# Performance work log

Hardware: AMD Instinct MI355X
Metric: run time of the kernel (lower is better)

The kernel has to match this reference:

```python
import jax, jax.numpy as jnp
import numpy as np

N = 50000   # nodes
E = 800000  # edges (avg degree 16)
D = 128     # dim (in == out per layer)
R = 8       # num_relations
B = 4       # num_bases
L = 2       # conv_layer_num
EPS = 1e-5      # LayerNorm eps
SLOPE = 0.2     # leaky_relu negative slope


def setup_inputs() -> dict:
    key = jax.random.key(0)
    ks = jax.random.split(key, 10)
    s = 0.05
    x = jax.random.normal(ks[0], (N, D), dtype=jnp.float32)
    edge_index = jax.random.randint(ks[1], (2, E), 0, N)
    edge_type = jax.random.randint(ks[2], (E,), 0, R)
    basis = jax.random.normal(ks[3], (L, B, D, D), dtype=jnp.float32) * s
    att_r = jax.random.normal(ks[4], (L, R, B), dtype=jnp.float32) * s
    att = jax.random.normal(ks[5], (L, 2 * D), dtype=jnp.float32) * s
    root = jax.random.normal(ks[6], (L, D, D), dtype=jnp.float32) * s
    bias = jax.random.normal(ks[7], (L, D), dtype=jnp.float32) * s
    ln_w = jnp.ones((L, D), dtype=jnp.float32)
    ln_b = jnp.zeros((L, D), dtype=jnp.float32)
    return {"x": x, "edge_index": edge_index, "edge_type": edge_type,
            "basis": basis, "att_r": att_r, "att": att, "root": root,
            "bias": bias, "ln_w": ln_w, "ln_b": ln_b}


def _gnn_layer(x, src, dst, et, basis, att_r, att, root, bias, ln_w, ln_b):
    # relation weights from bases: [R, D, D]
    w = jnp.einsum('rb,bio->rio', att_r, basis)
    # transform all nodes under all relations once, then gather per edge
    xw = jnp.einsum('ni,rio->rno', x, w)          # [R, N, D]
    x_j = xw[et, src]                              # [E, D] relation-specific src msg
    xr = x @ root                                  # [N, D] root transform
    x_i = xr[dst]                                  # [E, D]
    # attention: (cat[x_i, x_j] * att).sum(-1), leaky_relu, segment softmax by dst
    alpha = x_i @ att[:D] + x_j @ att[D:]          # [E]
    alpha = jnp.where(alpha > 0, alpha, SLOPE * alpha)
    amax = jax.ops.segment_max(alpha, dst, num_segments=N)
    amax = jnp.where(jnp.isfinite(amax), amax, 0.0)
    ex = jnp.exp(alpha - amax[dst])
    denom = jax.ops.segment_sum(ex, dst, num_segments=N)
    alpha = ex / (denom[dst] + 1e-16)
    # weighted scatter-add aggregation (dropout rate = 0 -> identity)
    aggr = jax.ops.segment_sum(x_j * alpha[:, None], dst, num_segments=N)  # [N, D]
    out = aggr + xr + bias
    # LayerNorm
    mu = out.mean(-1, keepdims=True)
    var = out.var(-1, keepdims=True)
    out = (out - mu) / jnp.sqrt(var + EPS) * ln_w + ln_b
    return jnp.tanh(out)


def reference(x, edge_index, edge_type, basis, att_r, att, root, bias, ln_w, ln_b):
    src, dst = edge_index[0], edge_index[1]
    states = []
    for l in range(L):
        x = _gnn_layer(x, src, dst, edge_type, basis[l], att_r[l], att[l],
                       root[l], bias[l], ln_w[l], ln_b[l])
        states.append(x)
    return (x, jnp.stack(states))
```

## Files before the change

kernel.cpp:

```cpp
#include <hip/hip_runtime.h>
#include <math.h>

#define D 128
#define NB 4
#define NR 8
#define NLAYER 2
#define KTOT 640
#define EPSV 1e-5f
#define SLOPE 0.2f
#define NBUK 32
#define BSHIFT 11

typedef __attribute__((ext_vector_type(8))) short short8;
typedef __attribute__((ext_vector_type(4))) float f32x4;
typedef __attribute__((ext_vector_type(2))) float f32x2;

__device__ __forceinline__ unsigned short f2bf(float f) {
  unsigned u = __float_as_uint(f);
  u += 0x7FFF + ((u >> 16) & 1);
  return (unsigned short)(u >> 16);
}

__device__ __forceinline__ float block_sum_128(float v, volatile float* scratch) {
#pragma unroll
  for (int off = 32; off > 0; off >>= 1) v += __shfl_xor(v, off);
  __syncthreads();
  if ((threadIdx.x & 63) == 0) scratch[threadIdx.x >> 6] = v;
  __syncthreads();
  return scratch[0] + scratch[1];
}

__global__ void hist_kernel(const int* __restrict__ dst, int* __restrict__ deg, int E) {
  int e = blockIdx.x * 256 + threadIdx.x;
  if (e < E) atomicAdd(&deg[dst[e]], 1);
}

__global__ void __launch_bounds__(1024) scan_kernel(const int* __restrict__ deg,
                                                    int* __restrict__ offs,
                                                    int* __restrict__ cur,
                                                    int* __restrict__ bcur, int n) {
  __shared__ int wsums[16];
  const int tid = threadIdx.x, lane = tid & 63, wid = tid >> 6;
  int carry = 0;
  for (int base = 0; base < n; base += 4096) {
    int i0 = base + tid * 4;
    int v0 = 0, v1 = 0, v2 = 0, v3 = 0;
    if (i0 + 3 < n) {
      int4 q = *(const int4*)(deg + i0);
      v0 = q.x; v1 = q.y; v2 = q.z; v3 = q.w;
    } else if (i0 < n) {
      v0 = deg[i0];
      if (i0 + 1 < n) v1 = deg[i0 + 1];
      if (i0 + 2 < n) v2 = deg[i0 + 2];
    }
    int tsum = v0 + v1 + v2 + v3;
    int x = tsum;
#pragma unroll
    for (int off = 1; off < 64; off <<= 1) {
      int y = __shfl_up(x, off);
      if (lane >= off) x += y;
    }
    if (lane == 63) wsums[wid] = x;
    __syncthreads();
    if (wid == 0) {
      int ws = (lane < 16) ? wsums[lane] : 0;
#pragma unroll
      for (int off = 1; off < 16; off <<= 1) {
        int y = __shfl_up(ws, off);
        if (lane >= off) ws += y;
      }
      if (lane < 16) wsums[lane] = ws;
    }
    __syncthreads();
    int prefix = carry + ((wid > 0) ? wsums[wid - 1] : 0) + x - tsum;
    int e0 = prefix, e1 = e0 + v0, e2 = e1 + v1, e3 = e2 + v2;
    if (i0 < n)     { offs[i0] = e0;     cur[i0] = e0; }
    if (i0 + 1 < n) { offs[i0 + 1] = e1; cur[i0 + 1] = e1; }
    if (i0 + 2 < n) { offs[i0 + 2] = e2; cur[i0 + 2] = e2; }
    if (i0 + 3 < n) { offs[i0 + 3] = e3; cur[i0 + 3] = e3; }
    int btot = wsums[15];
    __syncthreads();
    carry += btot;
  }
  if (tid == 0) offs[n] = carry;
  __syncthreads();
  if (tid < NBUK) {
    int idx = tid << BSHIFT;
    bcur[tid * 16] = offs[idx < n ? idx : n];
  }
}

__global__ void __launch_bounds__(1024) bucket_kernel(
    const int* __restrict__ src, const int* __restrict__ dst, const int* __restrict__ et,
    int* __restrict__ bcur, unsigned long long* __restrict__ ebuf, int E) {
  __shared__ int lcnt[NBUK];
  __shared__ int lbase[NBUK];
  const int tid = threadIdx.x;
  const int e = blockIdx.x * 1024 + tid;
  if (tid < NBUK) lcnt[tid] = 0;
  __syncthreads();
  int d = 0, b = 0, rank = 0;
  unsigned pk = 0;
  bool valid = e < E;
  if (valid) {
    d = dst[e];
    pk = (unsigned)src[e] | ((unsigned)et[e] << 16);
    b = d >> BSHIFT;
    rank = atomicAdd(&lcnt[b], 1);
  }
  __syncthreads();
  if (tid < NBUK && lcnt[tid] > 0) lbase[tid] = atomicAdd(&bcur[tid * 16], lcnt[tid]);
  __syncthreads();
  if (valid) ebuf[lbase[b] + rank] = ((unsigned long long)(unsigned)d << 32) | pk;
}

__global__ void scatter2_kernel(const unsigned long long* __restrict__ ebuf,
                                int* __restrict__ cur, unsigned* __restrict__ csr, int E) {
  int e = blockIdx.x * 256 + threadIdx.x;
  if (e < E) {
    unsigned long long r = ebuf[e];
    int d = (int)(r >> 32);
    int pos = atomicAdd(&cur[d], 1);
    csr[pos] = (unsigned)r;
  }
}

__global__ void __launch_bounds__(128) prep_w(const float* __restrict__ basis,
                                              const float* __restrict__ root,
                                              const float* __restrict__ att,
                                              unsigned short* __restrict__ BT0,
                                              unsigned short* __restrict__ BT1,
                                              float* __restrict__ av0, float* __restrict__ av1) {
  __shared__ float scratch[2];
  int k = blockIdx.x, l = 0;
  if (k >= KTOT) { k -= KTOT; l = 1; }
  const float* basis_l = basis + (size_t)l * NB * D * D;
  const float* root_l  = root + (size_t)l * D * D;
  const float* att_l   = att + (size_t)l * 2 * D;
  unsigned short* BT = l ? BT1 : BT0;
  float* av = l ? av1 : av0;
  const int o = threadIdx.x;
  float v = (k < 512) ? basis_l[(size_t)(k >> 7) * (D * D) + (size_t)(k & 127) * D + o]
                      : root_l[(size_t)(k - 512) * D + o];
  BT[(size_t)o * KTOT + k] = f2bf(v);
  float w = (k < 512) ? att_l[D + o] : att_l[o];
  float s = block_sum_128(v * w, scratch);
  if (o == 0) av[k] = s;
}

__global__ void __launch_bounds__(256) prep_xa(const float* __restrict__ x0,
                                               const float* __restrict__ av,
                                               unsigned short* __restrict__ ga,
                                               float* __restrict__ ai,
                                               float* __restrict__ ajb, int N, int Npad) {
  int n = blockIdx.x * 4 + (threadIdx.x >> 6);
  int lane = threadIdx.x & 63;
  if (n >= Npad) return;
  if (n >= N) {
    *(unsigned*)(ga + (size_t)n * KTOT + 512 + 2 * lane) = 0;
    return;
  }
  float2 xv = *(const float2*)(x0 + (size_t)n * D + 2 * lane);
  unsigned packed = (unsigned)f2bf(xv.x) | ((unsigned)f2bf(xv.y) << 16);
  *(unsigned*)(ga + (size_t)n * KTOT + 512 + 2 * lane) = packed;
  float d[5];
#pragma unroll
  for (int b = 0; b < 4; ++b) {
    float2 w = *(const float2*)(av + b * D + 2 * lane);
    d[b] = xv.x * w.x + xv.y * w.y;
  }
  {
    float2 w = *(const float2*)(av + 512 + 2 * lane);
    d[4] = xv.x * w.x + xv.y * w.y;
  }
#pragma unroll
  for (int off = 1; off < 64; off <<= 1) {
#pragma unroll
    for (int i = 0; i < 5; ++i) d[i] += __shfl_xor(d[i], off);
  }
  if (lane == 0) {
    *(float4*)(ajb + (size_t)n * 4) = make_float4(d[0], d[1], d[2], d[3]);
    ai[n] = d[4];
  }
}

__global__ void __launch_bounds__(256) node_flash(
    unsigned short* __restrict__ ga, const float* __restrict__ ai, const float* __restrict__ ajb,
    const int* __restrict__ offs, const unsigned* __restrict__ csr,
    const float* __restrict__ attr_l, int N) {
  __shared__ float s_c[NR * NB];
  __shared__ float4 s_wc[4][68];
  __shared__ unsigned s_pk[4][68];
  const int w = threadIdx.x >> 6, lane = threadIdx.x & 63;
  const int g = lane >> 4, s = lane & 15;
  const int gb = g * 17;
  const int n = blockIdx.x * 16 + w * 4 + g;
  if (lane < NR * NB) s_c[lane] = attr_l[lane];
  int b0 = 0, b1 = 0;
  float ain = 0.f;
  if (n < N) { b0 = offs[n]; b1 = offs[n + 1]; ain = ai[n]; }
  float ssum = 0.f;
  f32x2 acc[4][4];
#pragma unroll
  for (int b = 0; b < 4; ++b)
#pragma unroll
    for (int k = 0; k < 4; ++k) acc[b][k] = (f32x2){0.f, 0.f};

  int nch = (b1 - b0 + 15) >> 4;
  nch = max(nch, __shfl_xor(nch, 16));
  nch = max(nch, __shfl_xor(nch, 32));

  const unsigned short* gax = ga + 512u + (unsigned)s * 8u;

  for (int ch = 0; ch < nch; ++ch) {
    const int cb = b0 + (ch << 4);
    const int cnt = min(16, b1 - cb);
    float4 wc = make_float4(0.f, 0.f, 0.f, 0.f);
    unsigned pk = 0;
    if (s < cnt) {
      pk = csr[cb + s];
      unsigned sn = pk & 0xFFFFu, rt = pk >> 16;
      float4 aj = *(const float4*)(ajb + (size_t)sn * 4);
      float4 cv = *(const float4*)(&s_c[rt * 4]);
      float a = ain + cv.x * aj.x + cv.y * aj.y + cv.z * aj.z + cv.w * aj.w;
      a = fmaxf(a, SLOPE * a);
      float ex = __expf(a);
      ssum += ex;
      wc = make_float4(ex * cv.x, ex * cv.y, ex * cv.z, ex * cv.w);
    }
    s_pk[w][gb + s] = pk;
    s_wc[w][gb + s] = wc;
    int cc = max(cnt, 0);
    cc = max(cc, __shfl_xor(cc, 16));
    cc = max(cc, __shfl_xor(cc, 32));
    const float4* wrow = &s_wc[w][gb];
    const unsigned* prow = &s_pk[w][gb];
#pragma unroll 4
    for (int j = 0; j < cc; ++j) {
      float4 wcj = wrow[j];
      unsigned sn = prow[j] & 0xFFFFu;
      const uint4 q = *(const uint4*)(gax + sn * (unsigned)KTOT);
      f32x2 W0 = {wcj.x, wcj.x}, W1 = {wcj.y, wcj.y};
      f32x2 W2 = {wcj.z, wcj.z}, W3 = {wcj.w, wcj.w};
#define ACC2(K, QQ) { \
      f32x2 X = { __uint_as_float((QQ) << 16), __uint_as_float((QQ) & 0xFFFF0000u) }; \
      acc[0][K] = __builtin_elementwise_fma(W0, X, acc[0][K]); \
      acc[1][K] = __builtin_elementwise_fma(W1, X, acc[1][K]); \
      acc[2][K] = __builtin_elementwise_fma(W2, X, acc[2][K]); \
      acc[3][K] = __builtin_elementwise_fma(W3, X, acc[3][K]); }
      ACC2(0, q.x) ACC2(1, q.y) ACC2(2, q.z) ACC2(3, q.w)
#undef ACC2
    }
  }
#pragma unroll
  for (int off = 1; off < 16; off <<= 1) ssum += __shfl_xor(ssum, off);
  if (n < N) {
    const float inv = 1.f / (ssum + 1e-16f);
    unsigned short* gp = ga + (size_t)n * KTOT;
#pragma unroll
    for (int b = 0; b < 4; ++b) {
      uint4 r;
      r.x = (unsigned)f2bf(acc[b][0].x * inv) | ((unsigned)f2bf(acc[b][0].y * inv) << 16);
      r.y = (unsigned)f2bf(acc[b][1].x * inv) | ((unsigned)f2bf(acc[b][1].y * inv) << 16);
      r.z = (unsigned)f2bf(acc[b][2].x * inv) | ((unsigned)f2bf(acc[b][2].y * inv) << 16);
      r.w = (unsigned)f2bf(acc[b][3].x * inv) | ((unsigned)f2bf(acc[b][3].y * inv) << 16);
      *(uint4*)(gp + b * D + s * 8) = r;
    }
  }
}

__global__ void __launch_bounds__(512) gemm2_kernel(
    unsigned short* __restrict__ ga, const unsigned short* __restrict__ BT,
    const float* __restrict__ bias_l, const float* __restrict__ lnw_l,
    const float* __restrict__ lnb_l, float* __restrict__ st,
    float* __restrict__ xfinal, const float* __restrict__ avp,
    float* __restrict__ ai, float* __restrict__ ajb, int n_nodes) {
  __shared__ unsigned short sB[128 * 72];
  const int tid = threadIdx.x;
  const int wv = tid >> 6, lane = tid & 63;
  const int l15 = lane & 15, quad = lane >> 4;
  const int rowb = blockIdx.x * 128 + wv * 16;
  const unsigned short* garow = ga + (size_t)(rowb + l15) * KTOT;
  f32x4 acc[8];
  const f32x4 zero = {0.f, 0.f, 0.f, 0.f};
#pragma unroll
  for (int ct = 0; ct < 8; ++ct) acc[ct] = zero;
#pragma unroll
  for (int ch = 0; ch < 10; ++ch) {
    const int k0 = ch * 64;
    short8 a[2];
#pragma unroll
    for (int kc = 0; kc < 2; ++kc)
      a[kc] = *(const short8*)(garow + k0 + kc * 32 + quad * 8);
    __syncthreads();
#pragma unroll
    for (int p = 0; p < 2; ++p) {
      int idx = p * 512 + tid;
      int col = idx >> 3, k8 = idx & 7;
      *(short8*)(sB + col * 72 + k8 * 8) =
          *(const short8*)(BT + (size_t)col * KTOT + k0 + k8 * 8);
    }
    __syncthreads();
#pragma unroll
    for (int kc = 0; kc < 2; ++kc) {
#pragma unroll
      for (int ct = 0; ct < 8; ++ct) {
        const short8* b = (const short8*)(sB + (ct * 16 + l15) * 72 + kc * 32 + quad * 8);
        acc[ct] = __builtin_amdgcn_mfma_f32_16x16x32_bf16(a[kc], *b, acc[ct], 0, 0, 0);
      }
    }
  }
  const int r0 = rowb + quad * 4;
  float bia[8], lw[8], lb[8];
#pragma unroll
  for (int ct = 0; ct < 8; ++ct) {
    int col = ct * 16 + l15;
    bia[ct] = bias_l[col]; lw[ct] = lnw_l[col]; lb[ct] = lnb_l[col];
  }
  float vsum[4] = {0.f, 0.f, 0.f, 0.f}, vsq[4] = {0.f, 0.f, 0.f, 0.f};
#pragma unroll
  for (int ct = 0; ct < 8; ++ct) {
#pragma unroll
    for (int r = 0; r < 4; ++r) {
      float v = acc[ct][r] + bia[ct];
      acc[ct][r] = v;
      vsum[r] += v; vsq[r] += v * v;
    }
  }
#pragma unroll
  for (int r = 0; r < 4; ++r) {
#pragma unroll
    for (int off = 1; off < 16; off <<= 1) {
      vsum[r] += __shfl_xor(vsum[r], off);
      vsq[r]  += __shfl_xor(vsq[r], off);
    }
  }
  float mu[4], rs[4];
#pragma unroll
  for (int r = 0; r < 4; ++r) {
    mu[r] = vsum[r] * (1.0f / D);
    float var = vsq[r] * (1.0f / D) - mu[r] * mu[r];
    rs[r] = rsqrtf(var + EPSV);
  }
  float part[4][5];
#pragma unroll
  for (int r = 0; r < 4; ++r)
#pragma unroll
    for (int b = 0; b < 5; ++b) part[r][b] = 0.f;
#pragma unroll
  for (int ct = 0; ct < 8; ++ct) {
    int col = ct * 16 + l15;
    float a0 = 0.f, a1 = 0.f, a2v = 0.f, a3 = 0.f, a4 = 0.f;
    if (avp) {
      a0 = avp[col]; a1 = avp[D + col]; a2v = avp[2 * D + col];
      a3 = avp[3 * D + col]; a4 = avp[4 * D + col];
    }
#pragma unroll
    for (int r = 0; r < 4; ++r) {
      int row = r0 + r;
      if (row >= n_nodes) continue;
      float nv = (acc[ct][r] - mu[r]) * rs[r] * lw[ct] + lb[ct];
      float val = tanhf(nv);
      st[(size_t)row * D + col] = val;
      if (xfinal) xfinal[(size_t)row * D + col] = val;
      ga[(size_t)row * KTOT + 512 + col] = f2bf(val);
      if (avp) {
        part[r][0] = fmaf(val, a0, part[r][0]);
        part[r][1] = fmaf(val, a1, part[r][1]);
        part[r][2] = fmaf(val, a2v, part[r][2]);
        part[r][3] = fmaf(val, a3, part[r][3]);
        part[r][4] = fmaf(val, a4, part[r][4]);
      }
    }
  }
  if (avp) {
#pragma unroll
    for (int off = 1; off < 16; off <<= 1)
#pragma unroll
      for (int r = 0; r < 4; ++r)
#pragma unroll
        for (int b = 0; b < 5; ++b) part[r][b] += __shfl_xor(part[r][b], off);
    if (l15 == 0) {
#pragma unroll
      for (int r = 0; r < 4; ++r) {
        int row = r0 + r;
        if (row < n_nodes) {
          *(float4*)(ajb + (size_t)row * 4) =
              make_float4(part[r][0], part[r][1], part[r][2], part[r][3]);
          ai[row] = part[r][4];
        }
      }
    }
  }
}

extern "C" void kernel_launch(void* const* d_in, const int* in_sizes, int n_in,
                              void* d_out, int out_size, void* d_ws, size_t ws_size,
                              hipStream_t stream) {
  const float* x0    = (const float*)d_in[0];
  const int*   ei    = (const int*)d_in[1];
  const int*   etype = (const int*)d_in[2];
  const float* basis = (const float*)d_in[3];
  const float* att_r = (const float*)d_in[4];
  const float* att   = (const float*)d_in[5];
  const float* root  = (const float*)d_in[6];
  const float* bias  = (const float*)d_in[7];
  const float* lnw   = (const float*)d_in[8];
  const float* lnb   = (const float*)d_in[9];
  float* out = (float*)d_out;
  const int N = in_sizes[0] / D;
  const int E = in_sizes[2];
  const int Npad = ((N + 127) / 128) * 128;

  char* p = (char*)d_ws;
  auto alloc = [&](size_t bytes) { void* r = (void*)p; p += (bytes + 255) & ~(size_t)255; return r; };
  unsigned short*     ga   = (unsigned short*)alloc((size_t)Npad * KTOT * 2);
  unsigned short*     BT0  = (unsigned short*)alloc((size_t)D * KTOT * 2);
  unsigned short*     BT1  = (unsigned short*)alloc((size_t)D * KTOT * 2);
  float*              av0  = (float*)alloc((size_t)KTOT * 4);
  float*              av1  = (float*)alloc((size_t)KTOT * 4);
  float*              ai   = (float*)alloc((size_t)N * 4);
  float*              ajb  = (float*)alloc((size_t)N * 4 * 4);
  int*                deg  = (int*)alloc((size_t)N * 4);
  int*                offs = (int*)alloc((size_t)(N + 1) * 4);
  int*                cur  = (int*)alloc((size_t)N * 4);
  int*                bcur = (int*)alloc((size_t)NBUK * 16 * 4);
  unsigned*           csr  = (unsigned*)alloc((size_t)E * 4);
  unsigned long long* ebuf = (unsigned long long*)alloc((size_t)E * 8);

  const int* srcp = ei;
  const int* dstp = ei + E;

  hipMemsetAsync(deg, 0, (size_t)N * 4, stream);
  hist_kernel<<<(E + 255) / 256, 256, 0, stream>>>(dstp, deg, E);
  scan_kernel<<<1, 1024, 0, stream>>>(deg, offs, cur, bcur, N);
  bucket_kernel<<<(E + 1023) / 1024, 1024, 0, stream>>>(srcp, dstp, etype, bcur, ebuf, E);
  scatter2_kernel<<<(E + 255) / 256, 256, 0, stream>>>(ebuf, cur, csr, E);

  prep_w<<<2 * KTOT, 128, 0, stream>>>(basis, root, att, BT0, BT1, av0, av1);
  prep_xa<<<Npad / 4, 256, 0, stream>>>(x0, av0, ga, ai, ajb, N, Npad);

  float* states = out + (size_t)N * D;
  for (int l = 0; l < NLAYER; ++l) {
    const unsigned short* BT_l = l ? BT1 : BT0;
    node_flash<<<(N + 15) / 16, 256, 0, stream>>>(ga, ai, ajb, offs, csr,
                                                  att_r + (size_t)l * NR * NB, N);
    float* st = states + (size_t)l * N * D;
    gemm2_kernel<<<Npad / 128, 512, 0, stream>>>(ga, BT_l, bias + (size_t)l * D,
                                                 lnw + (size_t)l * D, lnb + (size_t)l * D,
                                                 st, (l == NLAYER - 1) ? out : nullptr,
                                                 (l == 0) ? av1 : nullptr, ai, ajb, N);
  }
}
```

Measured before the change: 392.8 us.

## Fuse prep kernels into graph-build launches and batch node_flash gathers

Merges weight preparation with the degree histogram, and the feature preparation with the prefix scan, cutting the launch count from six preprocessing kernels to four. In the merged scan kernel, block 0 runs the serial scan while the remaining blocks of 1024 threads handle the node features. node_flash now processes four 16-node tiles per block, and its edge loop is unrolled by four with all four row gathers issued before their FMAs to expose more memory-level parallelism. The trade-offs are more register pressure, padded iterations that read zero-weight slots, and a single-block scan that still serializes inside a larger grid.

Measured after the change: 380.3 us. 3.2% less time.

```diff
diff --git a/kernel.cpp b/kernel.cpp
--- a/kernel.cpp
+++ b/kernel.cpp
@@ -21,72 +21,130 @@
   return (unsigned short)(u >> 16);
 }
 
-__device__ __forceinline__ float block_sum_128(float v, volatile float* scratch) {
-#pragma unroll
-  for (int off = 32; off > 0; off >>= 1) v += __shfl_xor(v, off);
-  __syncthreads();
-  if ((threadIdx.x & 63) == 0) scratch[threadIdx.x >> 6] = v;
-  __syncthreads();
-  return scratch[0] + scratch[1];
-}
-
-__global__ void hist_kernel(const int* __restrict__ dst, int* __restrict__ deg, int E) {
-  int e = blockIdx.x * 256 + threadIdx.x;
-  if (e < E) atomicAdd(&deg[dst[e]], 1);
-}
-
-__global__ void __launch_bounds__(1024) scan_kernel(const int* __restrict__ deg,
-                                                    int* __restrict__ offs,
-                                                    int* __restrict__ cur,
-                                                    int* __restrict__ bcur, int n) {
+__global__ void __launch_bounds__(256) prepw_hist(
+    const float* __restrict__ basis, const float* __restrict__ root,
+    const float* __restrict__ att,
+    unsigned short* __restrict__ BT0, unsigned short* __restrict__ BT1,
+    float* __restrict__ av0, float* __restrict__ av1,
+    const int* __restrict__ dst, int* __restrict__ deg, int E) {
+  const int tid = threadIdx.x, lane = tid & 63, wid = tid >> 6;
+  if (blockIdx.x < (2 * KTOT) / 4) {
+    const int kk = blockIdx.x * 4 + wid;
+    const int l = kk >= KTOT ? 1 : 0;
+    const int k = kk - l * KTOT;
+    const float* basis_l = basis + (size_t)l * NB * D * D;
+    const float* root_l  = root + (size_t)l * D * D;
+    const float* att_l   = att + (size_t)l * 2 * D;
+    unsigned short* BT = l ? BT1 : BT0;
+    float* av = l ? av1 : av0;
+    const int o = lane;
+    float v1, v2, w1, w2;
+    if (k < 512) {
+      const float* bp = basis_l + (size_t)(k >> 7) * (D * D) + (size_t)(k & 127) * D;
+      v1 = bp[o]; v2 = bp[o + 64];
+      w1 = att_l[D + o]; w2 = att_l[D + o + 64];
+    } else {
+      const float* rp = root_l + (size_t)(k - 512) * D;
+      v1 = rp[o]; v2 = rp[o + 64];
+      w1 = att_l[o]; w2 = att_l[o + 64];
+    }
+    BT[(size_t)o * KTOT + k] = f2bf(v1);
+    BT[(size_t)(o + 64) * KTOT + k] = f2bf(v2);
+    float sv = v1 * w1 + v2 * w2;
+#pragma unroll
+    for (int off = 32; off > 0; off >>= 1) sv += __shfl_xor(sv, off);
+    if (lane == 0) av[k] = sv;
+  }
+  const int gtid = blockIdx.x * 256 + tid;
+  const int nthr = gridDim.x * 256;
+  for (int e = gtid; e < E; e += nthr) atomicAdd(&deg[dst[e]], 1);
+}
+
+__global__ void __launch_bounds__(1024) scan_prepxa(
+    const int* __restrict__ deg, int* __restrict__ offs, int* __restrict__ cur,
+    int* __restrict__ bcur, int n,
+    const float* __restrict__ x0, const float* __restrict__ av,
+    unsigned short* __restrict__ ga, float* __restrict__ ai, float* __restrict__ ajb,
+    int N, int Npad) {
   __shared__ int wsums[16];
   const int tid = threadIdx.x, lane = tid & 63, wid = tid >> 6;
-  int carry = 0;
-  for (int base = 0; base < n; base += 4096) {
-    int i0 = base + tid * 4;
-    int v0 = 0, v1 = 0, v2 = 0, v3 = 0;
-    if (i0 + 3 < n) {
-      int4 q = *(const int4*)(deg + i0);
-      v0 = q.x; v1 = q.y; v2 = q.z; v3 = q.w;
-    } else if (i0 < n) {
-      v0 = deg[i0];
-      if (i0 + 1 < n) v1 = deg[i0 + 1];
-      if (i0 + 2 < n) v2 = deg[i0 + 2];
-    }
-    int tsum = v0 + v1 + v2 + v3;
-    int x = tsum;
-#pragma unroll
-    for (int off = 1; off < 64; off <<= 1) {
-      int y = __shfl_up(x, off);
-      if (lane >= off) x += y;
-    }
-    if (lane == 63) wsums[wid] = x;
+  if (blockIdx.x == 0) {
+    int carry = 0;
+    for (int base = 0; base < n; base += 4096) {
+      int i0 = base + tid * 4;
+      int v0 = 0, v1 = 0, v2 = 0, v3 = 0;
+      if (i0 + 3 < n) {
+        int4 q = *(const int4*)(deg + i0);
+        v0 = q.x; v1 = q.y; v2 = q.z; v3 = q.w;
+      } else if (i0 < n) {
+        v0 = deg[i0];
+        if (i0 + 1 < n) v1 = deg[i0 + 1];
+        if (i0 + 2 < n) v2 = deg[i0 + 2];
+      }
+      int tsum = v0 + v1 + v2 + v3;
+      int x = tsum;
+#pragma unroll
+      for (int off = 1; off < 64; off <<= 1) {
+        int y = __shfl_up(x, off);
+        if (lane >= off) x += y;
+      }
+      if (lane == 63) wsums[wid] = x;
+      __syncthreads();
+      if (wid == 0) {
+        int ws = (lane < 16) ? wsums[lane] : 0;
+#pragma unroll
+        for (int off = 1; off < 16; off <<= 1) {
+          int y = __shfl_up(ws, off);
+          if (lane >= off) ws += y;
+        }
+        if (lane < 16) wsums[lane] = ws;
+      }
+      __syncthreads();
+      int prefix = carry + ((wid > 0) ? wsums[wid - 1] : 0) + x - tsum;
+      int e0 = prefix, e1 = e0 + v0, e2 = e1 + v1, e3 = e2 + v2;
+      if (i0 < n)     { offs[i0] = e0;     cur[i0] = e0; }
+      if (i0 + 1 < n) { offs[i0 + 1] = e1; cur[i0 + 1] = e1; }
+      if (i0 + 2 < n) { offs[i0 + 2] = e2; cur[i0 + 2] = e2; }
+      if (i0 + 3 < n) { offs[i0 + 3] = e3; cur[i0 + 3] = e3; }
+      int btot = wsums[15];
+      __syncthreads();
+      carry += btot;
+    }
+    if (tid == 0) offs[n] = carry;
     __syncthreads();
-    if (wid == 0) {
-      int ws = (lane < 16) ? wsums[lane] : 0;
-#pragma unroll
-      for (int off = 1; off < 16; off <<= 1) {
-        int y = __shfl_up(ws, off);
-        if (lane >= off) ws += y;
-      }
-      if (lane < 16) wsums[lane] = ws;
-    }
-    __syncthreads();
-    int prefix = carry + ((wid > 0) ? wsums[wid - 1] : 0) + x - tsum;
-    int e0 = prefix, e1 = e0 + v0, e2 = e1 + v1, e3 = e2 + v2;
-    if (i0 < n)     { offs[i0] = e0;     cur[i0] = e0; }
-    if (i0 + 1 < n) { offs[i0 + 1] = e1; cur[i0 + 1] = e1; }
-    if (i0 + 2 < n) { offs[i0 + 2] = e2; cur[i0 + 2] = e2; }
-    if (i0 + 3 < n) { offs[i0 + 3] = e3; cur[i0 + 3] = e3; }
-    int btot = wsums[15];
-    __syncthreads();
-    carry += btot;
-  }
-  if (tid == 0) offs[n] = carry;
-  __syncthreads();
-  if (tid < NBUK) {
-    int idx = tid << BSHIFT;
-    bcur[tid * 16] = offs[idx < n ? idx : n];
+    if (tid < NBUK) {
+      int idx = tid << BSHIFT;
+      bcur[tid * 16] = offs[idx < n ? idx : n];
+    }
+    return;
+  }
+  const int nn = (blockIdx.x - 1) * 16 + wid;
+  if (nn >= Npad) return;
+  if (nn >= N) {
+    *(unsigned*)(ga + (size_t)nn * KTOT + 512 + 2 * lane) = 0;
+    return;
+  }
+  float2 xv = *(const float2*)(x0 + (size_t)nn * D + 2 * lane);
+  unsigned packed = (unsigned)f2bf(xv.x) | ((unsigned)f2bf(xv.y) << 16);
+  *(unsigned*)(ga + (size_t)nn * KTOT + 512 + 2 * lane) = packed;
+  float d[5];
+#pragma unroll
+  for (int b = 0; b < 4; ++b) {
+    float2 w = *(const float2*)(av + b * D + 2 * lane);
+    d[b] = xv.x * w.x + xv.y * w.y;
+  }
+  {
+    float2 w = *(const float2*)(av + 512 + 2 * lane);
+    d[4] = xv.x * w.x + xv.y * w.y;
+  }
+#pragma unroll
+  for (int off = 1; off < 64; off <<= 1) {
+#pragma unroll
+    for (int i = 0; i < 5; ++i) d[i] += __shfl_xor(d[i], off);
+  }
+  if (lane == 0) {
+    *(float4*)(ajb + (size_t)nn * 4) = make_float4(d[0], d[1], d[2], d[3]);
+    ai[nn] = d[4];
   }
 }
 
@@ -125,65 +183,6 @@
   }
 }
 
-__global__ void __launch_bounds__(128) prep_w(const float* __restrict__ basis,
-                                              const float* __restrict__ root,
-                                              const float* __restrict__ att,
-                                              unsigned short* __restrict__ BT0,
-                                              unsigned short* __restrict__ BT1,
-                                              float* __restrict__ av0, float* __restrict__ av1) {
-  __shared__ float scratch[2];
-  int k = blockIdx.x, l = 0;
-  if (k >= KTOT) { k -= KTOT; l = 1; }
-  const float* basis_l = basis + (size_t)l * NB * D * D;
-  const float* root_l  = root + (size_t)l * D * D;
-  const float* att_l   = att + (size_t)l * 2 * D;
-  unsigned short* BT = l ? BT1 : BT0;
-  float* av = l ? av1 : av0;
-  const int o = threadIdx.x;
-  float v = (k < 512) ? basis_l[(size_t)(k >> 7) * (D * D) + (size_t)(k & 127) * D + o]
-                      : root_l[(size_t)(k - 512) * D + o];
-  BT[(size_t)o * KTOT + k] = f2bf(v);
-  float w = (k < 512) ? att_l[D + o] : att_l[o];
-  float s = block_sum_128(v * w, scratch);
-  if (o == 0) av[k] = s;
-}
-
-__global__ void __launch_bounds__(256) prep_xa(const float* __restrict__ x0,
-                                               const float* __restrict__ av,
-                                               unsigned short* __restrict__ ga,
-                                               float* __restrict__ ai,
-                                               float* __restrict__ ajb, int N, int Npad) {
-  int n = blockIdx.x * 4 + (threadIdx.x >> 6);
-  int lane = threadIdx.x & 63;
-  if (n >= Npad) return;
-  if (n >= N) {
-    *(unsigned*)(ga + (size_t)n * KTOT + 512 + 2 * lane) = 0;
-    return;
-  }
-  float2 xv = *(const float2*)(x0 + (size_t)n * D + 2 * lane);
-  unsigned packed = (unsigned)f2bf(xv.x) | ((unsigned)f2bf(xv.y) << 16);
-  *(unsigned*)(ga + (size_t)n * KTOT + 512 + 2 * lane) = packed;
-  float d[5];
-#pragma unroll
-  for (int b = 0; b < 4; ++b) {
-    float2 w = *(const float2*)(av + b * D + 2 * lane);
-    d[b] = xv.x * w.x + xv.y * w.y;
-  }
-  {
-    float2 w = *(const float2*)(av + 512 + 2 * lane);
-    d[4] = xv.x * w.x + xv.y * w.y;
-  }
-#pragma unroll
-  for (int off = 1; off < 64; off <<= 1) {
-#pragma unroll
-    for (int i = 0; i < 5; ++i) d[i] += __shfl_xor(d[i], off);
-  }
-  if (lane == 0) {
-    *(float4*)(ajb + (size_t)n * 4) = make_float4(d[0], d[1], d[2], d[3]);
-    ai[n] = d[4];
-  }
-}
-
 __global__ void __launch_bounds__(256) node_flash(
     unsigned short* __restrict__ ga, const float* __restrict__ ai, const float* __restrict__ ajb,
     const int* __restrict__ offs, const unsigned* __restrict__ csr,
@@ -194,77 +193,100 @@
   const int w = threadIdx.x >> 6, lane = threadIdx.x & 63;
   const int g = lane >> 4, s = lane & 15;
   const int gb = g * 17;
-  const int n = blockIdx.x * 16 + w * 4 + g;
   if (lane < NR * NB) s_c[lane] = attr_l[lane];
-  int b0 = 0, b1 = 0;
-  float ain = 0.f;
-  if (n < N) { b0 = offs[n]; b1 = offs[n + 1]; ain = ai[n]; }
-  float ssum = 0.f;
-  f32x2 acc[4][4];
-#pragma unroll
-  for (int b = 0; b < 4; ++b)
-#pragma unroll
-    for (int k = 0; k < 4; ++k) acc[b][k] = (f32x2){0.f, 0.f};
-
-  int nch = (b1 - b0 + 15) >> 4;
-  nch = max(nch, __shfl_xor(nch, 16));
-  nch = max(nch, __shfl_xor(nch, 32));
-
   const unsigned short* gax = ga + 512u + (unsigned)s * 8u;
-
-  for (int ch = 0; ch < nch; ++ch) {
-    const int cb = b0 + (ch << 4);
-    const int cnt = min(16, b1 - cb);
-    float4 wc = make_float4(0.f, 0.f, 0.f, 0.f);
-    unsigned pk = 0;
-    if (s < cnt) {
-      pk = csr[cb + s];
-      unsigned sn = pk & 0xFFFFu, rt = pk >> 16;
-      float4 aj = *(const float4*)(ajb + (size_t)sn * 4);
-      float4 cv = *(const float4*)(&s_c[rt * 4]);
-      float a = ain + cv.x * aj.x + cv.y * aj.y + cv.z * aj.z + cv.w * aj.w;
-      a = fmaxf(a, SLOPE * a);
-      float ex = __expf(a);
-      ssum += ex;
-      wc = make_float4(ex * cv.x, ex * cv.y, ex * cv.z, ex * cv.w);
-    }
-    s_pk[w][gb + s] = pk;
-    s_wc[w][gb + s] = wc;
-    int cc = max(cnt, 0);
-    cc = max(cc, __shfl_xor(cc, 16));
-    cc = max(cc, __shfl_xor(cc, 32));
-    const float4* wrow = &s_wc[w][gb];
-    const unsigned* prow = &s_pk[w][gb];
-#pragma unroll 4
-    for (int j = 0; j < cc; ++j) {
-      float4 wcj = wrow[j];
-      unsigned sn = prow[j] & 0xFFFFu;
-      const uint4 q = *(const uint4*)(gax + sn * (unsigned)KTOT);
-      f32x2 W0 = {wcj.x, wcj.x}, W1 = {wcj.y, wcj.y};
-      f32x2 W2 = {wcj.z, wcj.z}, W3 = {wcj.w, wcj.w};
-#define ACC2(K, QQ) { \
-      f32x2 X = { __uint_as_float((QQ) << 16), __uint_as_float((QQ) & 0xFFFF0000u) }; \
-      acc[0][K] = __builtin_elementwise_fma(W0, X, acc[0][K]); \
-      acc[1][K] = __builtin_elementwise_fma(W1, X, acc[1][K]); \
-      acc[2][K] = __builtin_elementwise_fma(W2, X, acc[2][K]); \
-      acc[3][K] = __builtin_elementwise_fma(W3, X, acc[3][K]); }
-      ACC2(0, q.x) ACC2(1, q.y) ACC2(2, q.z) ACC2(3, q.w)
-#undef ACC2
-    }
-  }
-#pragma unroll
-  for (int off = 1; off < 16; off <<= 1) ssum += __shfl_xor(ssum, off);
-  if (n < N) {
-    const float inv = 1.f / (ssum + 1e-16f);
-    unsigned short* gp = ga + (size_t)n * KTOT;
-#pragma unroll
-    for (int b = 0; b < 4; ++b) {
-      uint4 r;
-      r.x = (unsigned)f2bf(acc[b][0].x * inv) | ((unsigned)f2bf(acc[b][0].y * inv) << 16);
-      r.y = (unsigned)f2bf(acc[b][1].x * inv) | ((unsigned)f2bf(acc[b][1].y * inv) << 16);
-      r.z = (unsigned)f2bf(acc[b][2].x * inv) | ((unsigned)f2bf(acc[b][2].y * inv) << 16);
-      r.w = (unsigned)f2bf(acc[b][3].x * inv) | ((unsigned)f2bf(acc[b][3].y * inv) << 16);
-      *(uint4*)(gp + b * D + s * 8) = r;
+  const int base0 = blockIdx.x * 64;
+
+  for (int t = 0; t < 4; ++t) {
+    const int n = base0 + t * 16 + w * 4 + g;
+    int b0 = 0, b1 = 0;
+    float ain = 0.f;
+    if (n < N) { b0 = offs[n]; b1 = offs[n + 1]; ain = ai[n]; }
+    float ssum = 0.f;
+    f32x2 acc[4][4];
+#pragma unroll
+    for (int b = 0; b < 4; ++b)
+#pragma unroll
+      for (int k = 0; k < 4; ++k) acc[b][k] = (f32x2){0.f, 0.f};
+
+    int nch = (b1 - b0 + 15) >> 4;
+    nch = max(nch, __shfl_xor(nch, 16));
+    nch = max(nch, __shfl_xor(nch, 32));
+
+    for (int ch = 0; ch < nch; ++ch) {
+      const int cb = b0 + (ch << 4);
+      const int cnt = min(16, b1 - cb);
+      float4 wc = make_float4(0.f, 0.f, 0.f, 0.f);
+      unsigned pk = 0;
+      if (s < cnt) {
+        pk = csr[cb + s];
+        unsigned sn = pk & 0xFFFFu, rt = pk >> 16;
+        float4 aj = *(const float4*)(ajb + (size_t)sn * 4);
+        float4 cv = *(const float4*)(&s_c[rt * 4]);
+        float a = ain + cv.x * aj.x + cv.y * aj.y + cv.z * aj.z + cv.w * aj.w;
+        a = fmaxf(a, SLOPE * a);
+        float ex = __expf(a);
+        ssum += ex;
+        wc = make_float4(ex * cv.x, ex * cv.y, ex * cv.z, ex * cv.w);
+      }
+      s_pk[w][gb + s] = pk;
+      s_wc[w][gb + s] = wc;
+      int cc = max(cnt, 0);
+      cc = max(cc, __shfl_xor(cc, 16));
+      cc = max(cc, __shfl_xor(cc, 32));
+      cc = (cc + 3) & ~3;
+      const float4* wrow = &s_wc[w][gb];
+      const unsigned* prow = &s_pk[w][gb];
+#define ACCROW(WC, QQ) { \
+      f32x2 W0 = {(WC).x, (WC).x}, W1 = {(WC).y, (WC).y}; \
+      f32x2 W2 = {(WC).z, (WC).z}, W3 = {(WC).w, (WC).w}; \
+      f32x2 X0 = { __uint_as_float((QQ).x << 16), __uint_as_float((QQ).x & 0xFFFF0000u) }; \
+      f32x2 X1 = { __uint_as_float((QQ).y << 16), __uint_as_float((QQ).y & 0xFFFF0000u) }; \
+      f32x2 X2 = { __uint_as_float((QQ).z << 16), __uint_as_float((QQ).z & 0xFFFF0000u) }; \
+      f32x2 X3 = { __uint_as_float((QQ).w << 16), __uint_as_float((QQ).w & 0xFFFF0000u) }; \
+      acc[0][0] = __builtin_elementwise_fma(W0, X0, acc[0][0]); \
+      acc[0][1] = __builtin_elementwise_fma(W0, X1, acc[0][1]); \
+      acc[0][2] = __builtin_elementwise_fma(W0, X2, acc[0][2]); \
+      acc[0][3] = __builtin_elementwise_fma(W0, X3, acc[0][3]); \
+      acc[1][0] = __builtin_elementwise_fma(W1, X0, acc[1][0]); \
+      acc[1][1] = __builtin_elementwise_fma(W1, X1, acc[1][1]); \
+      acc[1][2] = __builtin_elementwise_fma(W1, X2, acc[1][2]); \
+      acc[1][3] = __builtin_elementwise_fma(W1, X3, acc[1][3]); \
+      acc[2][0] = __builtin_elementwise_fma(W2, X0, acc[2][0]); \
+      acc[2][1] = __builtin_elementwise_fma(W2, X1, acc[2][1]); \
+      acc[2][2] = __builtin_elementwise_fma(W2, X2, acc[2][2]); \
+      acc[2][3] = __builtin_elementwise_fma(W2, X3, acc[2][3]); \
+      acc[3][0] = __builtin_elementwise_fma(W3, X0, acc[3][0]); \
+      acc[3][1] = __builtin_elementwise_fma(W3, X1, acc[3][1]); \
+      acc[3][2] = __builtin_elementwise_fma(W3, X2, acc[3][2]); \
+      acc[3][3] = __builtin_elementwise_fma(W3, X3, acc[3][3]); }
+      for (int jb = 0; jb < cc; jb += 4) {
+        float4 wa = wrow[jb + 0], wb = wrow[jb + 1];
+        float4 wcv = wrow[jb + 2], wd = wrow[jb + 3];
+        unsigned pa = prow[jb + 0], pb = prow[jb + 1];
+        unsigned pc = prow[jb + 2], pd = prow[jb + 3];
+        const uint4 qa = *(const uint4*)(gax + (pa & 0xFFFFu) * (unsigned)KTOT);
+        const uint4 qb = *(const uint4*)(gax + (pb & 0xFFFFu) * (unsigned)KTOT);
+        const uint4 qc = *(const uint4*)(gax + (pc & 0xFFFFu) * (unsigned)KTOT);
+        const uint4 qd = *(const uint4*)(gax + (pd & 0xFFFFu) * (unsigned)KTOT);
+        ACCROW(wa, qa) ACCROW(wb, qb) ACCROW(wcv, qc) ACCROW(wd, qd)
+      }
+#undef ACCROW
+    }
+#pragma unroll
+    for (int off = 1; off < 16; off <<= 1) ssum += __shfl_xor(ssum, off);
+    if (n < N) {
+      const float inv = 1.f / (ssum + 1e-16f);
+      unsigned short* gp = ga + (size_t)n * KTOT;
+#pragma unroll
+      for (int b = 0; b < 4; ++b) {
+        uint4 r;
+        r.x = (unsigned)f2bf(acc[b][0].x * inv) | ((unsigned)f2bf(acc[b][0].y * inv) << 16);
+        r.y = (unsigned)f2bf(acc[b][1].x * inv) | ((unsigned)f2bf(acc[b][1].y * inv) << 16);
+        r.z = (unsigned)f2bf(acc[b][2].x * inv) | ((unsigned)f2bf(acc[b][2].y * inv) << 16);
+        r.w = (unsigned)f2bf(acc[b][3].x * inv) | ((unsigned)f2bf(acc[b][3].y * inv) << 16);
+        *(uint4*)(gp + b * D + s * 8) = r;
+      }
     }
   }
 }
@@ -432,18 +454,17 @@
   const int* dstp = ei + E;
 
   hipMemsetAsync(deg, 0, (size_t)N * 4, stream);
-  hist_kernel<<<(E + 255) / 256, 256, 0, stream>>>(dstp, deg, E);
-  scan_kernel<<<1, 1024, 0, stream>>>(deg, offs, cur, bcur, N);
+  prepw_hist<<<320 + (E + 255) / 256, 256, 0, stream>>>(basis, root, att, BT0, BT1,
+                                                        av0, av1, dstp, deg, E);
+  scan_prepxa<<<1 + Npad / 16, 1024, 0, stream>>>(deg, offs, cur, bcur, N,
+                                                  x0, av0, ga, ai, ajb, N, Npad);
   bucket_kernel<<<(E + 1023) / 1024, 1024, 0, stream>>>(srcp, dstp, etype, bcur, ebuf, E);
   scatter2_kernel<<<(E + 255) / 256, 256, 0, stream>>>(ebuf, cur, csr, E);
-
-  prep_w<<<2 * KTOT, 128, 0, stream>>>(basis, root, att, BT0, BT1, av0, av1);
-  prep_xa<<<Npad / 4, 256, 0, stream>>>(x0, av0, ga, ai, ajb, N, Npad);
 
   float* states = out + (size_t)N * D;
   for (int l = 0; l < NLAYER; ++l) {
     const unsigned short* BT_l = l ? BT1 : BT0;
-    node_flash<<<(N + 15) / 16, 256, 0, stream>>>(ga, ai, ajb, offs, csr,
+    node_flash<<<(N + 63) / 64, 256, 0, stream>>>(ga, ai, ajb, offs, csr,
                                                   att_r + (size_t)l * NR * NB, N);
     float* st = states + (size_t)l * N * D;
     gemm2_kernel<<<Npad / 128, 512, 0, stream>>>(ga, BT_l, bias + (size_t)l * D,
```
